# Optimization experiments

Measured on AMD Instinct MI355X. Metric: run time of the kernel, lower is better.

The kernel has to match this reference:

```python
import jax, jax.numpy as jnp
import numpy as np

N, C, H, W = 2048, 16, 32, 32
E = 16384


def _conv(x, w, b):
    # 3x3 conv, stride 1, padding 1, NCHW/OIHW
    y = jax.lax.conv_general_dilated(
        x, w, window_strides=(1, 1), padding=((1, 1), (1, 1)),
        dimension_numbers=('NCHW', 'OIHW', 'NCHW'))
    return y + b[None, :, None, None]


def _get_nodes(fv, edges, positive):
    # fv: [N,C,H,W]; edges: [E,3] = (a, rel, b)
    rel = edges[:, 1]
    m = (rel > 0) if positive else (rel < 0)
    wmask = m.astype(fv.dtype)[:, None, None, None]  # [E,1,1,1]
    a = edges[:, 0]
    b = edges[:, 2]
    # symmetric scatter_add: fv[a] -> b and fv[b] -> a (masked edges contribute 0)
    nodes = jnp.zeros_like(fv)
    nodes = nodes.at[b].add(fv[a] * wmask)
    nodes = nodes.at[a].add(fv[b] * wmask)
    return nodes


def setup_inputs() -> dict:
    key = jax.random.key(0)
    ks = jax.random.split(key, 10)
    x = jax.random.normal(ks[0], (N, C, H, W), dtype=jnp.float32)
    ids = jax.random.randint(ks[1], (E, 2), 0, N)
    rel = jnp.where(jax.random.bernoulli(ks[2], 0.5, (E,)), 1, -1).astype(jnp.int64)
    edges = jnp.stack([ids[:, 0].astype(jnp.int64), rel, ids[:, 1].astype(jnp.int64)], axis=1)
    s = 0.05
    w1 = jax.random.normal(ks[3], (32, 48, 3, 3), dtype=jnp.float32) * s
    b1 = jax.random.normal(ks[4], (32,), dtype=jnp.float32) * s
    w2 = jax.random.normal(ks[5], (32, 32, 3, 3), dtype=jnp.float32) * s
    b2 = jax.random.normal(ks[6], (32,), dtype=jnp.float32) * s
    w3 = jax.random.normal(ks[7], (16, 32, 3, 3), dtype=jnp.float32) * s
    b3 = jax.random.normal(ks[8], (16,), dtype=jnp.float32) * s
    return {"x": x, "edges": edges, "w1": w1, "b1": b1, "w2": w2, "b2": b2, "w3": w3, "b3": b3}


def reference(x, edges, w1, b1, w2, b2, w3, b3):
    neigh = _get_nodes(x, edges, True)
    non_neigh = _get_nodes(x, edges, False)
    enc = jnp.concatenate([x, neigh, non_neigh], axis=1)  # [N,48,H,W]
    h = _conv(enc, w1, b1)
    h = _conv(h, w2, b2)
    return _conv(h, w3, b3)  # [N,16,H,W]
```

## Files before the change

kernel.cpp:

```cpp
#include <hip/hip_runtime.h>


#define NNODES 2048
#define HW 1024
#define PLANE 16384
#define CAP 128

typedef float v4f __attribute__((ext_vector_type(4)));
typedef short v8s __attribute__((ext_vector_type(8)));

__device__ inline unsigned short f2bfu(float f) {
    unsigned u = __float_as_uint(f);
    u += 0x7fffu + ((u >> 16) & 1u);
    return (unsigned short)(u >> 16);
}
__device__ inline unsigned pk2(float a, float b) {
    return (unsigned)f2bfu(a) | ((unsigned)f2bfu(b) << 16);
}
__device__ inline void add2(float& a, float& b, unsigned u) {
    a += __uint_as_float(u << 16);
    b += __uint_as_float(u & 0xffff0000u);
}

__global__ __launch_bounds__(256) void build_lists(
    const int* __restrict__ edges, int E, int* __restrict__ cnt, int* __restrict__ lists)
{
    int e = blockIdx.x * 256 + threadIdx.x;
    if (e >= E) return;
    int a = edges[3 * e + 0];
    int rel = edges[3 * e + 1];
    int b = edges[3 * e + 2];
    int s = (rel > 0) ? 0 : 1;
    int slot = atomicAdd(&cnt[b * 2 + s], 1);
    if (slot < CAP) lists[((size_t)(b * 2 + s)) * CAP + slot] = a;
    slot = atomicAdd(&cnt[a * 2 + s], 1);
    if (slot < CAP) lists[((size_t)(a * 2 + s)) * CAP + slot] = b;
}

__global__ __launch_bounds__(256) void xpose_bf16(
    const float* __restrict__ x, ushort* __restrict__ xb)
{
    int n = blockIdx.x, t = threadIdx.x;
    const float4* src = (const float4*)(x + (size_t)n * PLANE);
    float vv[64];
#pragma unroll
    for (int i = 0; i < 16; i++) {
        float4 v = src[i * 256 + t];
        vv[i * 4 + 0] = v.x; vv[i * 4 + 1] = v.y; vv[i * 4 + 2] = v.z; vv[i * 4 + 3] = v.w;
    }
    uint4* dst = (uint4*)(xb + (size_t)n * HW * 16);
#pragma unroll
    for (int j = 0; j < 4; j++) {
        uint4 o0, o1;
        o0.x = pk2(vv[0 * 4 + j], vv[1 * 4 + j]);
        o0.y = pk2(vv[2 * 4 + j], vv[3 * 4 + j]);
        o0.z = pk2(vv[4 * 4 + j], vv[5 * 4 + j]);
        o0.w = pk2(vv[6 * 4 + j], vv[7 * 4 + j]);
        o1.x = pk2(vv[8 * 4 + j], vv[9 * 4 + j]);
        o1.y = pk2(vv[10 * 4 + j], vv[11 * 4 + j]);
        o1.z = pk2(vv[12 * 4 + j], vv[13 * 4 + j]);
        o1.w = pk2(vv[14 * 4 + j], vv[15 * 4 + j]);
        dst[(4 * t + j) * 2 + 0] = o0;
        dst[(4 * t + j) * 2 + 1] = o1;
    }
}

__global__ __launch_bounds__(256) void gather_enc(
    const ushort* __restrict__ xb, const int* __restrict__ cnt,
    const int* __restrict__ lists, ushort* __restrict__ enc)
{
    int v = blockIdx.x, t = threadIdx.x;
    __shared__ int slist[2 * CAP];
    __shared__ int sdeg[2];
    if (t < 2) sdeg[t] = min(cnt[v * 2 + t], CAP);
    slist[t] = lists[(size_t)v * 2 * CAP + t];
    __syncthreads();

    uint4* edst = (uint4*)(enc + (size_t)v * HW * 64);
    const uint4* xsrc = (const uint4*)(xb + (size_t)v * HW * 16);
    const uint4 z = make_uint4(0, 0, 0, 0);
#pragma unroll
    for (int j = 0; j < 4; j++) {
        int q = 4 * t + j;
        edst[q * 8 + 0] = xsrc[q * 2 + 0];
        edst[q * 8 + 1] = xsrc[q * 2 + 1];
        edst[q * 8 + 6] = z;
        edst[q * 8 + 7] = z;
    }
    for (int s = 0; s < 2; s++) {
        float acc[64];
#pragma unroll
        for (int i = 0; i < 64; i++) acc[i] = 0.f;
        int d = sdeg[s];
        for (int k = 0; k < d; k++) {
            const uint4* sp = (const uint4*)(xb + (size_t)slist[s * CAP + k] * HW * 16);
#pragma unroll
            for (int j = 0; j < 4; j++) {
                uint4 p0 = sp[(4 * t + j) * 2 + 0];
                uint4 p1 = sp[(4 * t + j) * 2 + 1];
                add2(acc[j * 16 + 0],  acc[j * 16 + 1],  p0.x);
                add2(acc[j * 16 + 2],  acc[j * 16 + 3],  p0.y);
                add2(acc[j * 16 + 4],  acc[j * 16 + 5],  p0.z);
                add2(acc[j * 16 + 6],  acc[j * 16 + 7],  p0.w);
                add2(acc[j * 16 + 8],  acc[j * 16 + 9],  p1.x);
                add2(acc[j * 16 + 10], acc[j * 16 + 11], p1.y);
                add2(acc[j * 16 + 12], acc[j * 16 + 13], p1.z);
                add2(acc[j * 16 + 14], acc[j * 16 + 15], p1.w);
            }
        }
#pragma unroll
        for (int j = 0; j < 4; j++) {
            uint4 o0, o1;
            o0.x = pk2(acc[j * 16 + 0],  acc[j * 16 + 1]);
            o0.y = pk2(acc[j * 16 + 2],  acc[j * 16 + 3]);
            o0.z = pk2(acc[j * 16 + 4],  acc[j * 16 + 5]);
            o0.w = pk2(acc[j * 16 + 6],  acc[j * 16 + 7]);
            o1.x = pk2(acc[j * 16 + 8],  acc[j * 16 + 9]);
            o1.y = pk2(acc[j * 16 + 10], acc[j * 16 + 11]);
            o1.z = pk2(acc[j * 16 + 12], acc[j * 16 + 13]);
            o1.w = pk2(acc[j * 16 + 14], acc[j * 16 + 15]);
            edst[(4 * t + j) * 8 + 2 + s * 2 + 0] = o0;
            edst[(4 * t + j) * 8 + 2 + s * 2 + 1] = o1;
        }
    }
}

template<int CI_REAL, int KCH, int CO>
__global__ __launch_bounds__(256) void prep_wfrag(
    const float* __restrict__ wt, ushort* __restrict__ wf)
{
    const int total = (CO / 16) * 9 * KCH * 64;
    for (int idx = blockIdx.x * 256 + threadIdx.x; idx < total; idx += gridDim.x * 256) {
        int lane = idx & 63;
        int t = idx >> 6;
        int kc = t % KCH; t /= KCH;
        int khw = t % 9;  t /= 9;
        int cot = t;
        int nco = cot * 16 + (lane & 15);
        int kq  = lane >> 4;
        float w[8];
#pragma unroll
        for (int j = 0; j < 8; j++) {
            int k = kc * 32 + kq * 8 + j;
            w[j] = (k < CI_REAL) ? wt[((size_t)nco * CI_REAL + k) * 9 + khw] : 0.f;
        }
        uint4 o;
        o.x = pk2(w[0], w[1]); o.y = pk2(w[2], w[3]);
        o.z = pk2(w[4], w[5]); o.w = pk2(w[6], w[7]);
        *(uint4*)&wf[(size_t)idx * 8] = o;
    }
}

template<int CI_REAL, int CIP_G, int CIP_L, int KCH, int CO, bool OUT_F32>
__global__ __launch_bounds__(256) void conv_mfma(
    const ushort* __restrict__ in, const ushort* __restrict__ wf,
    const float* __restrict__ bias, ushort* __restrict__ outb,
    float* __restrict__ outf)
{
    __shared__ ushort tile[320 * CIP_L];
    const int n = blockIdx.x >> 2;
    const int r0 = (blockIdx.x & 3) * 8;
    const int CH4 = CIP_G / 8;

    const uint4* gsrc = (const uint4*)(in + (size_t)n * HW * CIP_G);
    for (int idx = threadIdx.x; idx < 320 * CH4; idx += 256) {
        int lp = idx / CH4;
        int ch = idx - lp * CH4;
        int gr = r0 - 1 + (lp >> 5);
        uint4 val = make_uint4(0, 0, 0, 0);
        if (gr >= 0 && gr < 32) val = gsrc[(size_t)(gr * 32 + (lp & 31)) * CH4 + ch];
        *(uint4*)&tile[lp * CIP_L + ch * 8] = val;
    }
    __syncthreads();

    const int wv = threadIdx.x >> 6;
    const int lane = threadIdx.x & 63;
    const int l15 = lane & 15;
    const int kq = lane >> 4;

    const int cotile = (CO == 32) ? (wv >> 1) : 0;
    const int cob = cotile * 16;
    const int nco = cob + l15;

    const v8s* wfv = (const v8s*)wf;
    v8s bfrag[9 * KCH];
#pragma unroll
    for (int khw = 0; khw < 9; khw++)
#pragma unroll
        for (int kc = 0; kc < KCH; kc++)
            bfrag[khw * KCH + kc] = wfv[(size_t)(((cotile * 9 + khw) * KCH + kc) * 64 + lane)];
    const float bv = bias[nco];

    int mt0, mtstep, nmt;
    if (CO == 32) { mt0 = wv & 1; mtstep = 2; nmt = 8; }
    else          { mt0 = wv;     mtstep = 4; nmt = 4; }

    for (int it = 0; it < nmt; it++) {
        int mtile = mt0 + it * mtstep;
        int r = r0 + (mtile >> 1);
        int c = (mtile & 1) * 16 + l15;
        v4f acc = {bv, bv, bv, bv};
#pragma unroll
        for (int khw = 0; khw < 9; khw++) {
            int dh = khw / 3 - 1, dw = (khw % 3) - 1;
            int rr = r + dh;
            if (rr < 0 || rr > 31) continue;
            int cc = c + dw;
            bool okc = (cc >= 0) && (cc <= 31);
            int lp = (rr - r0 + 1) * 32 + (okc ? cc : 0);
#pragma unroll
            for (int kc = 0; kc < KCH; kc++) {
                v8s a = *(const v8s*)&tile[lp * CIP_L + kc * 32 + kq * 8];
                if (!okc) a = (v8s)0;
                acc = __builtin_amdgcn_mfma_f32_16x16x32_bf16(a, bfrag[khw * KCH + kc], acc, 0, 0, 0);
            }
        }
        int pbase = r * 32 + (mtile & 1) * 16 + kq * 4;
        if (OUT_F32) {
            float4 o; o.x = acc[0]; o.y = acc[1]; o.z = acc[2]; o.w = acc[3];
            *(float4*)(outf + ((size_t)n * CO + nco) * HW + pbase) = o;
        } else {
#pragma unroll
            for (int reg = 0; reg < 4; reg++)
                outb[((size_t)n * HW + pbase + reg) * CO + nco] = (ushort)f2bfu(acc[reg]);
        }
    }
}

extern "C" void kernel_launch(void* const* d_in, const int* in_sizes, int n_in,
                              void* d_out, int out_size, void* d_ws, size_t ws_size,
                              hipStream_t stream)
{
    const float* x     = (const float*)d_in[0];
    const int*   edges = (const int*)d_in[1];
    const float* w1    = (const float*)d_in[2];
    const float* b1    = (const float*)d_in[3];
    const float* w2    = (const float*)d_in[4];
    const float* b2    = (const float*)d_in[5];
    const float* w3    = (const float*)d_in[6];
    const float* b3    = (const float*)d_in[7];
    float* out = (float*)d_out;

    const int E = in_sizes[1] / 3;

    ushort* enc = (ushort*)d_ws;
    ushort* h1  = enc + (size_t)NNODES * HW * 64;
    ushort* xb  = h1  + (size_t)NNODES * HW * 32;
    int*    cnt   = (int*)(xb + (size_t)NNODES * HW * 16);
    int*    lists = cnt + NNODES * 2;
    ushort* wf1 = (ushort*)(lists + (size_t)NNODES * 2 * CAP);
    ushort* wf2 = wf1 + 2 * 9 * 2 * 64 * 8;
    ushort* wf3 = wf2 + 2 * 9 * 1 * 64 * 8;
    ushort* h2  = enc;

    hipMemsetAsync(cnt, 0, NNODES * 2 * sizeof(int), stream);
    build_lists<<<(E + 255) / 256, 256, 0, stream>>>(edges, E, cnt, lists);

    prep_wfrag<48, 2, 32><<<9, 256, 0, stream>>>(w1, wf1);
    prep_wfrag<32, 1, 32><<<5, 256, 0, stream>>>(w2, wf2);
    prep_wfrag<32, 1, 16><<<3, 256, 0, stream>>>(w3, wf3);

    xpose_bf16<<<NNODES, 256, 0, stream>>>(x, xb);
    gather_enc<<<NNODES, 256, 0, stream>>>(xb, cnt, lists, enc);

    conv_mfma<48, 64, 72, 2, 32, false><<<NNODES * 4, 256, 0, stream>>>(enc, wf1, b1, h1, nullptr);
    conv_mfma<32, 32, 40, 1, 32, false><<<NNODES * 4, 256, 0, stream>>>(h1, wf2, b2, h2, nullptr);
    conv_mfma<32, 32, 40, 1, 16, true><<<NNODES * 4, 256, 0, stream>>>(h2, wf3, b3, nullptr, out);
}
```

Measured before the change: 853.5 us.

## Slice neighbor gather by pixel and drop zero padding from encoding channels

The gather kernel is reorganised so each block handles 8 nodes times a 32-pixel slice, with one thread per pixel and 16 accumulators instead of 64. Block indices are ordered so blocks running together read the same pixel slice across many nodes, which should improve L2 locality for the random neighbor reads and raise occupancy. The encoding buffer shrinks from 64 to 48 channels, removing the zero-padding writes and reads. The first conv then masks out the out-of-range K lanes so it can still use two 32-wide K chunks, and pads the shared tile slightly so the over-read of the last pixel stays in bounds.

```diff
diff --git a/kernel.cpp b/kernel.cpp
--- a/kernel.cpp
+++ b/kernel.cpp
@@ -5,6 +5,9 @@
 #define HW 1024
 #define PLANE 16384
 #define CAP 128
+#define SLICE_PX 32
+#define NSLICE 32
+#define NPB 8
 
 typedef float v4f __attribute__((ext_vector_type(4)));
 typedef short v8s __attribute__((ext_vector_type(8)));
@@ -65,63 +68,52 @@
     }
 }
 
-__global__ __launch_bounds__(256) void gather_enc(
+__global__ __launch_bounds__(256) void gather_enc_slice(
     const ushort* __restrict__ xb, const int* __restrict__ cnt,
     const int* __restrict__ lists, ushort* __restrict__ enc)
 {
-    int v = blockIdx.x, t = threadIdx.x;
-    __shared__ int slist[2 * CAP];
-    __shared__ int sdeg[2];
-    if (t < 2) sdeg[t] = min(cnt[v * 2 + t], CAP);
-    slist[t] = lists[(size_t)v * 2 * CAP + t];
-    __syncthreads();
-
-    uint4* edst = (uint4*)(enc + (size_t)v * HW * 64);
-    const uint4* xsrc = (const uint4*)(xb + (size_t)v * HW * 16);
-    const uint4 z = make_uint4(0, 0, 0, 0);
-#pragma unroll
-    for (int j = 0; j < 4; j++) {
-        int q = 4 * t + j;
-        edst[q * 8 + 0] = xsrc[q * 2 + 0];
-        edst[q * 8 + 1] = xsrc[q * 2 + 1];
-        edst[q * 8 + 6] = z;
-        edst[q * 8 + 7] = z;
-    }
+    int idx = blockIdx.x;
+    int x8 = idx & 7;
+    int g  = (idx >> 3) & 255;
+    int p  = idx >> 11;
+    int slice = p * 8 + x8;
+    int t = threadIdx.x;
+    int node = g * NPB + (t >> 5);
+    int px = slice * SLICE_PX + (t & 31);
+
+    const uint4* xsrc = (const uint4*)(xb + ((size_t)node * HW + px) * 16);
+    uint4* edst = (uint4*)(enc + ((size_t)node * HW + px) * 48);
+    edst[0] = xsrc[0];
+    edst[1] = xsrc[1];
+
     for (int s = 0; s < 2; s++) {
-        float acc[64];
-#pragma unroll
-        for (int i = 0; i < 64; i++) acc[i] = 0.f;
-        int d = sdeg[s];
+        int d = min(cnt[node * 2 + s], CAP);
+        const int* lst = lists + (size_t)(node * 2 + s) * CAP;
+        float acc[16];
+#pragma unroll
+        for (int i = 0; i < 16; i++) acc[i] = 0.f;
+        int nb = (d > 0) ? lst[0] : 0;
         for (int k = 0; k < d; k++) {
-            const uint4* sp = (const uint4*)(xb + (size_t)slist[s * CAP + k] * HW * 16);
-#pragma unroll
-            for (int j = 0; j < 4; j++) {
-                uint4 p0 = sp[(4 * t + j) * 2 + 0];
-                uint4 p1 = sp[(4 * t + j) * 2 + 1];
-                add2(acc[j * 16 + 0],  acc[j * 16 + 1],  p0.x);
-                add2(acc[j * 16 + 2],  acc[j * 16 + 3],  p0.y);
-                add2(acc[j * 16 + 4],  acc[j * 16 + 5],  p0.z);
-                add2(acc[j * 16 + 6],  acc[j * 16 + 7],  p0.w);
-                add2(acc[j * 16 + 8],  acc[j * 16 + 9],  p1.x);
-                add2(acc[j * 16 + 10], acc[j * 16 + 11], p1.y);
-                add2(acc[j * 16 + 12], acc[j * 16 + 13], p1.z);
-                add2(acc[j * 16 + 14], acc[j * 16 + 15], p1.w);
-            }
-        }
-#pragma unroll
-        for (int j = 0; j < 4; j++) {
-            uint4 o0, o1;
-            o0.x = pk2(acc[j * 16 + 0],  acc[j * 16 + 1]);
-            o0.y = pk2(acc[j * 16 + 2],  acc[j * 16 + 3]);
-            o0.z = pk2(acc[j * 16 + 4],  acc[j * 16 + 5]);
-            o0.w = pk2(acc[j * 16 + 6],  acc[j * 16 + 7]);
-            o1.x = pk2(acc[j * 16 + 8],  acc[j * 16 + 9]);
-            o1.y = pk2(acc[j * 16 + 10], acc[j * 16 + 11]);
-            o1.z = pk2(acc[j * 16 + 12], acc[j * 16 + 13]);
-            o1.w = pk2(acc[j * 16 + 14], acc[j * 16 + 15]);
-            edst[(4 * t + j) * 8 + 2 + s * 2 + 0] = o0;
-            edst[(4 * t + j) * 8 + 2 + s * 2 + 1] = o1;
-        }
+            const uint4* sp = (const uint4*)(xb + ((size_t)nb * HW + px) * 16);
+            uint4 p0 = sp[0];
+            uint4 p1 = sp[1];
+            nb = (k + 1 < d) ? lst[k + 1] : 0;
+            add2(acc[0],  acc[1],  p0.x);
+            add2(acc[2],  acc[3],  p0.y);
+            add2(acc[4],  acc[5],  p0.z);
+            add2(acc[6],  acc[7],  p0.w);
+            add2(acc[8],  acc[9],  p1.x);
+            add2(acc[10], acc[11], p1.y);
+            add2(acc[12], acc[13], p1.z);
+            add2(acc[14], acc[15], p1.w);
+        }
+        uint4 o0, o1;
+        o0.x = pk2(acc[0],  acc[1]);  o0.y = pk2(acc[2],  acc[3]);
+        o0.z = pk2(acc[4],  acc[5]);  o0.w = pk2(acc[6],  acc[7]);
+        o1.x = pk2(acc[8],  acc[9]);  o1.y = pk2(acc[10], acc[11]);
+        o1.z = pk2(acc[12], acc[13]); o1.w = pk2(acc[14], acc[15]);
+        edst[2 + s * 2 + 0] = o0;
+        edst[2 + s * 2 + 1] = o1;
     }
 }
 
@@ -157,7 +149,7 @@
     const float* __restrict__ bias, ushort* __restrict__ outb,
     float* __restrict__ outf)
 {
-    __shared__ ushort tile[320 * CIP_L];
+    __shared__ ushort tile[320 * CIP_L + 8];
     const int n = blockIdx.x >> 2;
     const int r0 = (blockIdx.x & 3) * 8;
     const int CH4 = CIP_G / 8;
@@ -211,7 +203,8 @@
 #pragma unroll
             for (int kc = 0; kc < KCH; kc++) {
                 v8s a = *(const v8s*)&tile[lp * CIP_L + kc * 32 + kq * 8];
-                if (!okc) a = (v8s)0;
+                bool kok = (kc * 32 + 32 <= CI_REAL) || (kc * 32 + kq * 8 < CI_REAL);
+                if (!okc || !kok) a = (v8s)0;
                 acc = __builtin_amdgcn_mfma_f32_16x16x32_bf16(a, bfrag[khw * KCH + kc], acc, 0, 0, 0);
             }
         }
@@ -244,7 +237,7 @@
     const int E = in_sizes[1] / 3;
 
     ushort* enc = (ushort*)d_ws;
-    ushort* h1  = enc + (size_t)NNODES * HW * 64;
+    ushort* h1  = enc + (size_t)NNODES * HW * 48;
     ushort* xb  = h1  + (size_t)NNODES * HW * 32;
     int*    cnt   = (int*)(xb + (size_t)NNODES * HW * 16);
     int*    lists = cnt + NNODES * 2;
@@ -261,9 +254,9 @@
     prep_wfrag<32, 1, 16><<<3, 256, 0, stream>>>(w3, wf3);
 
     xpose_bf16<<<NNODES, 256, 0, stream>>>(x, xb);
-    gather_enc<<<NNODES, 256, 0, stream>>>(xb, cnt, lists, enc);
-
-    conv_mfma<48, 64, 72, 2, 32, false><<<NNODES * 4, 256, 0, stream>>>(enc, wf1, b1, h1, nullptr);
+    gather_enc_slice<<<NSLICE * (NNODES / NPB), 256, 0, stream>>>(xb, cnt, lists, enc);
+
+    conv_mfma<48, 48, 56, 2, 32, false><<<NNODES * 4, 256, 0, stream>>>(enc, wf1, b1, h1, nullptr);
     conv_mfma<32, 32, 40, 1, 32, false><<<NNODES * 4, 256, 0, stream>>>(h1, wf2, b2, h2, nullptr);
     conv_mfma<32, 32, 40, 1, 16, true><<<NNODES * 4, 256, 0, stream>>>(h2, wf3, b3, nullptr, out);
 }
```

New measurement: 694.5 us. 1.23x faster.
